# Optimization experiments

Hardware: AMD Instinct MI355X
Metric: run time of the kernel (lower is better)

Reference implementation:

```python
import jax, jax.numpy as jnp
import numpy as np

B, N, P = 8, 64, 128
DNODE, DEDGE, DEMB = 2048, 1024, 512
E = B * N * N


def setup_inputs() -> dict:
    key = jax.random.key(0)
    ks = jax.random.split(key, 12)
    x = jax.random.normal(ks[0], (B, N, DNODE), dtype=jnp.float32)
    interaction_feature = jax.random.normal(ks[1], (B, N, N, DEDGE), dtype=jnp.float32)
    s = 0.02
    W_phi = jax.random.normal(ks[2], (DNODE, DEMB), dtype=jnp.float32) * s
    b_phi = jax.random.normal(ks[3], (DEMB,), dtype=jnp.float32) * s
    W_psi = jax.random.normal(ks[4], (DNODE, DEMB), dtype=jnp.float32) * s
    b_psi = jax.random.normal(ks[5], (DEMB,), dtype=jnp.float32) * s
    W_node = jax.random.normal(ks[6], (DNODE, DEMB), dtype=jnp.float32) * s
    b_node = jax.random.normal(ks[7], (DEMB,), dtype=jnp.float32) * s
    W_rel = jax.random.normal(ks[8], (DEDGE, DEMB), dtype=jnp.float32) * s
    b_rel = jax.random.normal(ks[9], (DEMB,), dtype=jnp.float32) * s
    pairs = jax.random.randint(ks[10], (B, P, 2), 0, N, dtype=jnp.int32)
    # edge_locating_tensor: rows (batch, src, dst) covering the proposed edge set
    bb, ii, jj = jnp.meshgrid(jnp.arange(B), jnp.arange(N), jnp.arange(N), indexing='ij')
    edge_locating_tensor = jnp.stack([bb.ravel(), ii.ravel(), jj.ravel()], axis=1).astype(jnp.int32)  # [E,3]
    return {"x": x, "interaction_feature": interaction_feature, "W_phi": W_phi, "b_phi": b_phi,
            "W_psi": W_psi, "b_psi": b_psi, "W_node": W_node, "b_node": b_node,
            "W_rel": W_rel, "b_rel": b_rel, "pairs": pairs, "edge_locating_tensor": edge_locating_tensor}


def _lookup_edge(elt, b_idx, i0, i1):
    # boolean-mask argmax lookup, faithful to torch argmax(loc0*loc1*loc2)
    # elt: [E,3]; b_idx,i0,i1: [B,P] -> loc: [B,P] indices into edge list
    m = (elt[None, None, :, 0] == b_idx[:, :, None]) \
        & (elt[None, None, :, 1] == i0[:, :, None]) \
        & (elt[None, None, :, 2] == i1[:, :, None])  # [B,P,E]
    return jnp.argmax(m, axis=-1)


def reference(x, interaction_feature, W_phi, b_phi, W_psi, b_psi,
              W_node, b_node, W_rel, b_rel, pairs, edge_locating_tensor):
    # relationship proposal scoring: all-pairs einsum + sigmoid
    phi = x @ W_phi + b_phi                                    # [B,N,512]
    psi = x @ W_psi + b_psi                                    # [B,N,512]
    relatedness_score = jax.nn.sigmoid(jnp.einsum('bik,bjk->bij', phi, psi))  # [B,N,N]

    # node / relationship-node embedders
    node_emb = x @ W_node + b_node                             # [B,N,512]
    elt = edge_locating_tensor
    rel_feats = interaction_feature[elt[:, 0], elt[:, 1], elt[:, 2]]  # [E,1024] gather
    edge_emb = rel_feats @ W_rel + b_rel                       # [E,512]

    # classifier input construction (gather/argmax/scatter hot path, vectorized)
    ind0, ind1 = pairs[..., 0], pairs[..., 1]                  # [B,P]
    b_idx = jnp.broadcast_to(jnp.arange(B, dtype=jnp.int32)[:, None], ind0.shape)
    emb0 = node_emb[b_idx, ind0]                               # [B,P,512]
    emb1 = node_emb[b_idx, ind1]
    first_half = (emb0 + emb1) * 0.5                           # aggregate 'mean'

    loc_fwd = _lookup_edge(elt, b_idx, ind0, ind1)             # [B,P]
    loc_rev = _lookup_edge(elt, b_idx, ind1, ind0)
    e1 = edge_emb[loc_fwd]                                     # [B,P,512]
    e2 = edge_emb[loc_rev]
    second_half = (e1 + e2) * 0.5

    classifier_input = jnp.concatenate([first_half, second_half], axis=-1)  # [B,P,1024]
    return relatedness_score, classifier_input
```

## Files before the change

### kernel.cpp

```cpp
#include <hip/hip_runtime.h>
#include <hip/hip_bf16.h>


typedef _Float16 h16;
typedef h16 h16x4 __attribute__((ext_vector_type(4)));
typedef h16 h16x8 __attribute__((ext_vector_type(8)));
typedef float f32x4 __attribute__((ext_vector_type(4)));

static const long O_W3T  = 0;
static const long O_WREL = 6291456;
static const long O_XH   = 7340032;
static const long O_G    = 9437184;
static const long O_B3   = 11534336;
static const long O_YH   = 11540480;

__global__ __launch_bounds__(256) void k_prep(
    const float* __restrict__ Wphi, const float* __restrict__ Wpsi,
    const float* __restrict__ Wnode, const float* __restrict__ Wrel,
    const float* __restrict__ x, const float* __restrict__ bphi,
    const float* __restrict__ bpsi, const float* __restrict__ bnode,
    const float* __restrict__ feat, const int* __restrict__ pairs,
    h16* __restrict__ W3t, h16* __restrict__ Wrelt, h16* __restrict__ xh,
    float* __restrict__ b3, h16* __restrict__ G) {
  __shared__ float t[32][33];
  int bid = blockIdx.x, tid = threadIdx.x;
  if (bid < 3584) {
    const float* src; h16* dst; int K, tk, tn;
    if (bid < 3072) {
      int mat = bid >> 10, rem = bid & 1023;
      tk = rem >> 4; tn = rem & 15;
      src = mat == 0 ? Wphi : (mat == 1 ? Wpsi : Wnode);
      K = 2048; dst = W3t + (long)mat * 512 * 2048;
    } else {
      int rem = bid - 3072;
      tk = rem >> 4; tn = rem & 15;
      src = Wrel; K = 1024; dst = Wrelt;
    }
    {
      int row = tid >> 3, c4 = (tid & 7) * 4;
      float4 v = *(const float4*)(src + (long)(tk*32 + row)*512 + tn*32 + c4);
      t[row][c4+0] = v.x; t[row][c4+1] = v.y; t[row][c4+2] = v.z; t[row][c4+3] = v.w;
    }
    __syncthreads();
    {
      int n = tid >> 3, k4 = (tid & 7) * 4;
      h16x4 o = { (h16)t[k4+0][n], (h16)t[k4+1][n], (h16)t[k4+2][n], (h16)t[k4+3][n] };
      *(h16x4*)(dst + (long)(tn*32 + n)*K + tk*32 + k4) = o;
    }
  } else if (bid < 4102) {
    int b2 = bid - 3584;
    if (b2 < 512) {
      int idx = (b2*256 + tid) * 8;
      const float4* xv = (const float4*)(x + idx);
      float4 v0 = xv[0], v1 = xv[1];
      h16x8 o;
      o[0]=(h16)v0.x; o[1]=(h16)v0.y; o[2]=(h16)v0.z; o[3]=(h16)v0.w;
      o[4]=(h16)v1.x; o[5]=(h16)v1.y; o[6]=(h16)v1.z; o[7]=(h16)v1.w;
      *(h16x8*)(xh + idx) = o;
    } else {
      int i = (b2 - 512)*256 + tid;
      if (i < 1536) b3[i] = i < 512 ? bphi[i] : (i < 1024 ? bpsi[i-512] : bnode[i-1024]);
    }
  } else {
    int r = bid - 4102;
    int b = r >> 7;
    int i0 = pairs[r*2], i1 = pairs[r*2+1];
    const float4* f0 = (const float4*)(feat + (long)((b*64 + i0)*64 + i1) * 1024);
    const float4* f1 = (const float4*)(feat + (long)((b*64 + i1)*64 + i0) * 1024);
    float4 a = f0[tid], c = f1[tid];
    h16x4 o;
    o[0]=(h16)(0.5f*(a.x+c.x)); o[1]=(h16)(0.5f*(a.y+c.y));
    o[2]=(h16)(0.5f*(a.z+c.z)); o[3]=(h16)(0.5f*(a.w+c.w));
    *(h16x4*)(G + (long)r*1024 + tid*4) = o;
  }
}

__device__ __forceinline__ void mfma_compute(
    const h16 (*__restrict__ As)[72], const h16 (*__restrict__ Bs)[72],
    int wm, int wn, int fr, int kg, f32x4 acc[2][2]) {
#pragma unroll
  for (int kc = 0; kc < 2; ++kc) {
    int kb = kc*32 + kg;
    h16x8 fa0 = *(const h16x8*)&As[wm*32 + fr][kb];
    h16x8 fa1 = *(const h16x8*)&As[wm*32 + 16 + fr][kb];
    h16x8 fb0 = *(const h16x8*)&Bs[wn*32 + fr][kb];
    h16x8 fb1 = *(const h16x8*)&Bs[wn*32 + 16 + fr][kb];
    acc[0][0] = __builtin_amdgcn_mfma_f32_16x16x32_f16(fa0, fb0, acc[0][0], 0,0,0);
    acc[0][1] = __builtin_amdgcn_mfma_f32_16x16x32_f16(fa0, fb1, acc[0][1], 0,0,0);
    acc[1][0] = __builtin_amdgcn_mfma_f32_16x16x32_f16(fa1, fb0, acc[1][0], 0,0,0);
    acc[1][1] = __builtin_amdgcn_mfma_f32_16x16x32_f16(fa1, fb1, acc[1][1], 0,0,0);
  }
}

__device__ __forceinline__ void mfma_compute8(
    const h16 (*__restrict__ As)[72], const h16 (*__restrict__ Bs)[72],
    int wm, int wn, int fr, int kg, f32x4 acc[2]) {
#pragma unroll
  for (int kc = 0; kc < 2; ++kc) {
    int kb = kc*32 + kg;
    h16x8 fa0 = *(const h16x8*)&As[wm*32 + fr][kb];
    h16x8 fa1 = *(const h16x8*)&As[wm*32 + 16 + fr][kb];
    h16x8 fb  = *(const h16x8*)&Bs[wn*16 + fr][kb];
    acc[0] = __builtin_amdgcn_mfma_f32_16x16x32_f16(fa0, fb, acc[0], 0,0,0);
    acc[1] = __builtin_amdgcn_mfma_f32_16x16x32_f16(fa1, fb, acc[1], 0,0,0);
  }
}

#define BAR_LDS() { asm volatile("s_waitcnt lgkmcnt(0)" ::: "memory"); \
                    __builtin_amdgcn_s_barrier(); }

__global__ __launch_bounds__(512) void k_gemm(
    const h16* __restrict__ xh, const h16* __restrict__ W3t,
    const float* __restrict__ b3, h16* __restrict__ Yh,
    const h16* __restrict__ G, const h16* __restrict__ Wrelt,
    const float* __restrict__ brel, float* __restrict__ out) {
  __shared__ __align__(16) h16 As[2][64][72];
  __shared__ __align__(16) h16 Bs[2][64][72];
  int bid = blockIdx.x, tid = threadIdx.x;
  int lane = tid & 63, wave = tid >> 6;
  int wm = wave >> 2, wn = wave & 3;
  int srow = tid >> 3, skp = (tid & 7) * 8;
  int fr = lane & 15, kg = (lane >> 4) * 8;

  int isEdge = bid >= 192;
  int ntile = isEdge ? 2 : 1;
#pragma unroll 1
  for (int ti = 0; ti < ntile; ++ti) {
    if (ti) __syncthreads();
    const h16 *A, *Bt; int K, tileM, tileN;
    if (!isEdge) {
      A = xh; Bt = W3t; K = 2048;
      tileM = (bid / 24) * 64; tileN = (bid % 24) * 64;
    } else {
      int e = (bid - 192) * 2 + ti;
      A = G; Bt = Wrelt; K = 1024;
      tileM = (e >> 3) * 64; tileN = (e & 7) * 64;
    }
    const h16* Agp = A + (long)(tileM + srow) * K + skp;
    const h16* Bgp = Bt + (long)(tileN + srow) * K + skp;
    f32x4 acc[2] = {};

    h16x8 r0a = *(const h16x8*)(Agp);
    h16x8 r0b = *(const h16x8*)(Bgp);
    *(h16x8*)&As[0][srow][skp] = r0a;
    *(h16x8*)&Bs[0][srow][skp] = r0b;
    h16x8 ra1 = *(const h16x8*)(Agp + 64),  rb1 = *(const h16x8*)(Bgp + 64);
    h16x8 ra2 = *(const h16x8*)(Agp + 128), rb2 = *(const h16x8*)(Bgp + 128);
    BAR_LDS();
    int cur = 0;
#pragma unroll 1
    for (int k0 = 192; k0 < K; k0 += 64) {
      h16x8 raF = *(const h16x8*)(Agp + k0);
      h16x8 rbF = *(const h16x8*)(Bgp + k0);
      mfma_compute8(As[cur], Bs[cur], wm, wn, fr, kg, acc);
      *(h16x8*)&As[cur ^ 1][srow][skp] = ra1;
      *(h16x8*)&Bs[cur ^ 1][srow][skp] = rb1;
      BAR_LDS();
      ra1 = ra2; rb1 = rb2; ra2 = raF; rb2 = rbF;
      cur ^= 1;
    }
    mfma_compute8(As[cur], Bs[cur], wm, wn, fr, kg, acc);
    *(h16x8*)&As[cur ^ 1][srow][skp] = ra1;
    *(h16x8*)&Bs[cur ^ 1][srow][skp] = rb1;
    BAR_LDS();
    cur ^= 1;
    mfma_compute8(As[cur], Bs[cur], wm, wn, fr, kg, acc);
    *(h16x8*)&As[cur ^ 1][srow][skp] = ra2;
    *(h16x8*)&Bs[cur ^ 1][srow][skp] = rb2;
    BAR_LDS();
    cur ^= 1;
    mfma_compute8(As[cur], Bs[cur], wm, wn, fr, kg, acc);

    int r0 = 4 * (lane >> 4);
#pragma unroll
    for (int m = 0; m < 2; ++m) {
      int row = tileM + wm*32 + m*16 + r0;
      int col = tileN + wn*16 + fr;
      if (!isEdge) {
        float bb = b3[col];
#pragma unroll
        for (int r = 0; r < 4; ++r)
          Yh[(long)(row + r) * 1536 + col] = (h16)(acc[m][r] + bb);
      } else {
        float bb = brel[col];
#pragma unroll
        for (int r = 0; r < 4; ++r)
          out[32768 + 512 + (long)(row + r) * 1024 + col] = acc[m][r] + bb;
      }
    }
  }
}

#define GEMM_PIPELINE(Agp, Bgp, K)                                        \
  {                                                                       \
    h16x8 ra0 = *(const h16x8*)(Agp);                                     \
    h16x8 ra1 = *(const h16x8*)(Agp + 8);                                 \
    h16x8 rb0 = *(const h16x8*)(Bgp);                                     \
    h16x8 rb1 = *(const h16x8*)(Bgp + 8);                                 \
    *(h16x8*)&As[0][srow][skp]   = ra0;                                   \
    *(h16x8*)&As[0][srow][skp+8] = ra1;                                   \
    *(h16x8*)&Bs[0][srow][skp]   = rb0;                                   \
    *(h16x8*)&Bs[0][srow][skp+8] = rb1;                                   \
    __syncthreads();                                                      \
    int cur = 0;                                                          \
    for (int k0 = 64; k0 < (K); k0 += 64) {                               \
      ra0 = *(const h16x8*)(Agp + k0);                                    \
      ra1 = *(const h16x8*)(Agp + k0 + 8);                                \
      rb0 = *(const h16x8*)(Bgp + k0);                                    \
      rb1 = *(const h16x8*)(Bgp + k0 + 8);                                \
      mfma_compute(As[cur], Bs[cur], wm, wn, fr, kg, acc);                \
      int nxt = cur ^ 1;                                                  \
      *(h16x8*)&As[nxt][srow][skp]   = ra0;                               \
      *(h16x8*)&As[nxt][srow][skp+8] = ra1;                               \
      *(h16x8*)&Bs[nxt][srow][skp]   = rb0;                               \
      *(h16x8*)&Bs[nxt][srow][skp+8] = rb1;                               \
      __syncthreads();                                                    \
      cur = nxt;                                                          \
    }                                                                     \
    mfma_compute(As[cur], Bs[cur], wm, wn, fr, kg, acc);                  \
  }

__global__ __launch_bounds__(256) void k_epilogue(
    const h16* __restrict__ Yh, const int* __restrict__ pairs,
    float* __restrict__ out) {
  __shared__ __align__(16) h16 As[2][64][72];
  __shared__ __align__(16) h16 Bs[2][64][72];
  int bid = blockIdx.x, tid = threadIdx.x;
  if (bid < 8) {
    int lane = tid & 63, wave = tid >> 6;
    int wm = wave >> 1, wn = wave & 1;
    int srow = tid >> 2, skp = (tid & 3) * 16;
    int fr = lane & 15, kg = (lane >> 4) * 8;
    const h16* Ab = Yh + (long)bid * 64 * 1536;
    const h16* Agp = Ab + (long)srow * 1536 + skp;
    const h16* Bgp = Ab + (long)srow * 1536 + 512 + skp;
    f32x4 acc[2][2] = {};
    GEMM_PIPELINE(Agp, Bgp, 512);
    int r0 = 4 * (lane >> 4), c0 = lane & 15;
    float* ob = out + (long)bid * 4096;
#pragma unroll
    for (int m = 0; m < 2; ++m)
#pragma unroll
      for (int n = 0; n < 2; ++n) {
        int row = wm*32 + m*16 + r0;
        int col = wn*32 + n*16 + c0;
#pragma unroll
        for (int r = 0; r < 4; ++r) {
          float s = acc[m][n][r];
          ob[(long)(row + r) * 64 + col] = 1.f / (1.f + expf(-s));
        }
      }
  } else {
    int r = bid - 8;
    int b = r >> 7;
    int i0 = pairs[r*2], i1 = pairs[r*2+1];
    const h16* n0 = Yh + (long)(b*64 + i0)*1536 + 1024;
    const h16* n1 = Yh + (long)(b*64 + i1)*1536 + 1024;
    float* o = out + 32768 + (long)r*1024;
    for (int c = tid; c < 512; c += 256)
      o[c] = 0.5f*((float)n0[c] + (float)n1[c]);
  }
}

extern "C" void kernel_launch(void* const* d_in, const int* in_sizes, int n_in,
                              void* d_out, int out_size, void* d_ws, size_t ws_size,
                              hipStream_t stream) {
  const float* x     = (const float*)d_in[0];
  const float* feat  = (const float*)d_in[1];
  const float* Wphi  = (const float*)d_in[2];
  const float* bphi  = (const float*)d_in[3];
  const float* Wpsi  = (const float*)d_in[4];
  const float* bpsi  = (const float*)d_in[5];
  const float* Wnode = (const float*)d_in[6];
  const float* bnode = (const float*)d_in[7];
  const float* Wrel  = (const float*)d_in[8];
  const float* brel  = (const float*)d_in[9];
  const int*   pairs = (const int*)d_in[10];
  float* out = (float*)d_out;
  char* ws = (char*)d_ws;

  h16*   W3t   = (h16*)(ws + O_W3T);
  h16*   Wrelt = (h16*)(ws + O_WREL);
  h16*   xh    = (h16*)(ws + O_XH);
  h16*   G     = (h16*)(ws + O_G);
  float* b3    = (float*)(ws + O_B3);
  h16*   Yh    = (h16*)(ws + O_YH);

  k_prep<<<dim3(5126), dim3(256), 0, stream>>>(
      Wphi, Wpsi, Wnode, Wrel, x, bphi, bpsi, bnode, feat, pairs,
      W3t, Wrelt, xh, b3, G);
  k_gemm<<<dim3(256), dim3(512), 0, stream>>>(
      xh, W3t, b3, Yh, G, Wrelt, brel, out);
  k_epilogue<<<dim3(1032), dim3(256), 0, stream>>>(Yh, pairs, out);
}
```

Before: 34.80 us.

## Switch GEMM waves to intra-block split-K with LDS merge of partial accumulators

In the main GEMM and the relatedness einsum, the eight waves now form two K-slices of four waves each. Each wave computes a 32x32 sub-tile over half of every 64-wide K chunk instead of a 32x16 tile over the full chunk, which halves B-fragment reloads per MFMA. The two slices' partial sums are reduced through LDS before the epilogue. The einsum and gather epilogue kernel moves to 512 threads with the same split-K scheme. This adds two barriers and an LDS round trip per tile, and half the waves sit idle during the epilogue.

```diff
diff --git a/kernel.cpp b/kernel.cpp
--- a/kernel.cpp
+++ b/kernel.cpp
@@ -75,39 +75,80 @@
   }
 }
 
-__device__ __forceinline__ void mfma_compute(
+__device__ __forceinline__ void mfma4(
     const h16 (*__restrict__ As)[72], const h16 (*__restrict__ Bs)[72],
-    int wm, int wn, int fr, int kg, f32x4 acc[2][2]) {
-#pragma unroll
-  for (int kc = 0; kc < 2; ++kc) {
-    int kb = kc*32 + kg;
-    h16x8 fa0 = *(const h16x8*)&As[wm*32 + fr][kb];
-    h16x8 fa1 = *(const h16x8*)&As[wm*32 + 16 + fr][kb];
-    h16x8 fb0 = *(const h16x8*)&Bs[wn*32 + fr][kb];
-    h16x8 fb1 = *(const h16x8*)&Bs[wn*32 + 16 + fr][kb];
-    acc[0][0] = __builtin_amdgcn_mfma_f32_16x16x32_f16(fa0, fb0, acc[0][0], 0,0,0);
-    acc[0][1] = __builtin_amdgcn_mfma_f32_16x16x32_f16(fa0, fb1, acc[0][1], 0,0,0);
-    acc[1][0] = __builtin_amdgcn_mfma_f32_16x16x32_f16(fa1, fb0, acc[1][0], 0,0,0);
-    acc[1][1] = __builtin_amdgcn_mfma_f32_16x16x32_f16(fa1, fb1, acc[1][1], 0,0,0);
-  }
-}
-
-__device__ __forceinline__ void mfma_compute8(
-    const h16 (*__restrict__ As)[72], const h16 (*__restrict__ Bs)[72],
-    int wm, int wn, int fr, int kg, f32x4 acc[2]) {
-#pragma unroll
-  for (int kc = 0; kc < 2; ++kc) {
-    int kb = kc*32 + kg;
-    h16x8 fa0 = *(const h16x8*)&As[wm*32 + fr][kb];
-    h16x8 fa1 = *(const h16x8*)&As[wm*32 + 16 + fr][kb];
-    h16x8 fb  = *(const h16x8*)&Bs[wn*16 + fr][kb];
-    acc[0] = __builtin_amdgcn_mfma_f32_16x16x32_f16(fa0, fb, acc[0], 0,0,0);
-    acc[1] = __builtin_amdgcn_mfma_f32_16x16x32_f16(fa1, fb, acc[1], 0,0,0);
-  }
+    int wm, int wn, int kb, int fr, f32x4 acc[2][2]) {
+  h16x8 fa0 = *(const h16x8*)&As[wm*32 + fr][kb];
+  h16x8 fa1 = *(const h16x8*)&As[wm*32 + 16 + fr][kb];
+  h16x8 fb0 = *(const h16x8*)&Bs[wn*32 + fr][kb];
+  h16x8 fb1 = *(const h16x8*)&Bs[wn*32 + 16 + fr][kb];
+  acc[0][0] = __builtin_amdgcn_mfma_f32_16x16x32_f16(fa0, fb0, acc[0][0], 0,0,0);
+  acc[0][1] = __builtin_amdgcn_mfma_f32_16x16x32_f16(fa0, fb1, acc[0][1], 0,0,0);
+  acc[1][0] = __builtin_amdgcn_mfma_f32_16x16x32_f16(fa1, fb0, acc[1][0], 0,0,0);
+  acc[1][1] = __builtin_amdgcn_mfma_f32_16x16x32_f16(fa1, fb1, acc[1][1], 0,0,0);
 }
 
 #define BAR_LDS() { asm volatile("s_waitcnt lgkmcnt(0)" ::: "memory"); \
                     __builtin_amdgcn_s_barrier(); }
+
+template<int S>
+__device__ __forceinline__ void tile_splitk(
+    const h16* Agp, const h16* Bgp,
+    h16 (*As)[64][72], h16 (*Bs)[64][72],
+    int srow, int skp, int wm, int wn, int kb, int fr,
+    f32x4 acc[2][2]) {
+  h16x8 r0a = *(const h16x8*)(Agp);
+  h16x8 r0b = *(const h16x8*)(Bgp);
+  *(h16x8*)&As[0][srow][skp] = r0a;
+  *(h16x8*)&Bs[0][srow][skp] = r0b;
+  h16x8 ra1 = *(const h16x8*)(Agp + 64),  rb1 = *(const h16x8*)(Bgp + 64);
+  h16x8 ra2 = *(const h16x8*)(Agp + 128), rb2 = *(const h16x8*)(Bgp + 128);
+  BAR_LDS();
+  int cur = 0;
+#pragma unroll 1
+  for (int k0 = 192; k0 < S * 64; k0 += 64) {
+    h16x8 raF = *(const h16x8*)(Agp + k0);
+    h16x8 rbF = *(const h16x8*)(Bgp + k0);
+    mfma4(As[cur], Bs[cur], wm, wn, kb, fr, acc);
+    *(h16x8*)&As[cur ^ 1][srow][skp] = ra1;
+    *(h16x8*)&Bs[cur ^ 1][srow][skp] = rb1;
+    BAR_LDS();
+    ra1 = ra2; rb1 = rb2; ra2 = raF; rb2 = rbF;
+    cur ^= 1;
+  }
+  mfma4(As[cur], Bs[cur], wm, wn, kb, fr, acc);
+  *(h16x8*)&As[cur ^ 1][srow][skp] = ra1;
+  *(h16x8*)&Bs[cur ^ 1][srow][skp] = rb1;
+  BAR_LDS();
+  cur ^= 1;
+  mfma4(As[cur], Bs[cur], wm, wn, kb, fr, acc);
+  *(h16x8*)&As[cur ^ 1][srow][skp] = ra2;
+  *(h16x8*)&Bs[cur ^ 1][srow][skp] = rb2;
+  BAR_LDS();
+  cur ^= 1;
+  mfma4(As[cur], Bs[cur], wm, wn, kb, fr, acc);
+}
+
+__device__ __forceinline__ void splitk_merge(
+    h16 (*As)[64][72], int wave, int lane, f32x4 acc[2][2]) {
+  float* mb = (float*)As;
+  __syncthreads();
+  if (wave >= 4) {
+    int mi = ((wave - 4) * 64 + lane) * 16;
+    *(f32x4*)&mb[mi +  0] = acc[0][0];
+    *(f32x4*)&mb[mi +  4] = acc[0][1];
+    *(f32x4*)&mb[mi +  8] = acc[1][0];
+    *(f32x4*)&mb[mi + 12] = acc[1][1];
+  }
+  __syncthreads();
+  if (wave < 4) {
+    int mi = (wave * 64 + lane) * 16;
+    acc[0][0] += *(const f32x4*)&mb[mi +  0];
+    acc[0][1] += *(const f32x4*)&mb[mi +  4];
+    acc[1][0] += *(const f32x4*)&mb[mi +  8];
+    acc[1][1] += *(const f32x4*)&mb[mi + 12];
+  }
+}
 
 __global__ __launch_bounds__(512) void k_gemm(
     const h16* __restrict__ xh, const h16* __restrict__ W3t,
@@ -118,9 +159,11 @@
   __shared__ __align__(16) h16 Bs[2][64][72];
   int bid = blockIdx.x, tid = threadIdx.x;
   int lane = tid & 63, wave = tid >> 6;
-  int wm = wave >> 2, wn = wave & 3;
+  int kslice = wave >> 2, wsub = wave & 3;
+  int wm = wsub >> 1, wn = wsub & 1;
   int srow = tid >> 3, skp = (tid & 7) * 8;
-  int fr = lane & 15, kg = (lane >> 4) * 8;
+  int fr = lane & 15, kb = kslice * 32 + (lane >> 4) * 8;
+  int r0 = 4 * (lane >> 4), c0 = lane & 15;
 
   int isEdge = bid >= 192;
   int ntile = isEdge ? 2 : 1;
@@ -138,89 +181,35 @@
     }
     const h16* Agp = A + (long)(tileM + srow) * K + skp;
     const h16* Bgp = Bt + (long)(tileN + srow) * K + skp;
-    f32x4 acc[2] = {};
-
-    h16x8 r0a = *(const h16x8*)(Agp);
-    h16x8 r0b = *(const h16x8*)(Bgp);
-    *(h16x8*)&As[0][srow][skp] = r0a;
-    *(h16x8*)&Bs[0][srow][skp] = r0b;
-    h16x8 ra1 = *(const h16x8*)(Agp + 64),  rb1 = *(const h16x8*)(Bgp + 64);
-    h16x8 ra2 = *(const h16x8*)(Agp + 128), rb2 = *(const h16x8*)(Bgp + 128);
-    BAR_LDS();
-    int cur = 0;
-#pragma unroll 1
-    for (int k0 = 192; k0 < K; k0 += 64) {
-      h16x8 raF = *(const h16x8*)(Agp + k0);
-      h16x8 rbF = *(const h16x8*)(Bgp + k0);
-      mfma_compute8(As[cur], Bs[cur], wm, wn, fr, kg, acc);
-      *(h16x8*)&As[cur ^ 1][srow][skp] = ra1;
-      *(h16x8*)&Bs[cur ^ 1][srow][skp] = rb1;
-      BAR_LDS();
-      ra1 = ra2; rb1 = rb2; ra2 = raF; rb2 = rbF;
-      cur ^= 1;
-    }
-    mfma_compute8(As[cur], Bs[cur], wm, wn, fr, kg, acc);
-    *(h16x8*)&As[cur ^ 1][srow][skp] = ra1;
-    *(h16x8*)&Bs[cur ^ 1][srow][skp] = rb1;
-    BAR_LDS();
-    cur ^= 1;
-    mfma_compute8(As[cur], Bs[cur], wm, wn, fr, kg, acc);
-    *(h16x8*)&As[cur ^ 1][srow][skp] = ra2;
-    *(h16x8*)&Bs[cur ^ 1][srow][skp] = rb2;
-    BAR_LDS();
-    cur ^= 1;
-    mfma_compute8(As[cur], Bs[cur], wm, wn, fr, kg, acc);
-
-    int r0 = 4 * (lane >> 4);
-#pragma unroll
-    for (int m = 0; m < 2; ++m) {
-      int row = tileM + wm*32 + m*16 + r0;
-      int col = tileN + wn*16 + fr;
-      if (!isEdge) {
-        float bb = b3[col];
-#pragma unroll
-        for (int r = 0; r < 4; ++r)
-          Yh[(long)(row + r) * 1536 + col] = (h16)(acc[m][r] + bb);
-      } else {
-        float bb = brel[col];
-#pragma unroll
-        for (int r = 0; r < 4; ++r)
-          out[32768 + 512 + (long)(row + r) * 1024 + col] = acc[m][r] + bb;
-      }
-    }
-  }
-}
-
-#define GEMM_PIPELINE(Agp, Bgp, K)                                        \
-  {                                                                       \
-    h16x8 ra0 = *(const h16x8*)(Agp);                                     \
-    h16x8 ra1 = *(const h16x8*)(Agp + 8);                                 \
-    h16x8 rb0 = *(const h16x8*)(Bgp);                                     \
-    h16x8 rb1 = *(const h16x8*)(Bgp + 8);                                 \
-    *(h16x8*)&As[0][srow][skp]   = ra0;                                   \
-    *(h16x8*)&As[0][srow][skp+8] = ra1;                                   \
-    *(h16x8*)&Bs[0][srow][skp]   = rb0;                                   \
-    *(h16x8*)&Bs[0][srow][skp+8] = rb1;                                   \
-    __syncthreads();                                                      \
-    int cur = 0;                                                          \
-    for (int k0 = 64; k0 < (K); k0 += 64) {                               \
-      ra0 = *(const h16x8*)(Agp + k0);                                    \
-      ra1 = *(const h16x8*)(Agp + k0 + 8);                                \
-      rb0 = *(const h16x8*)(Bgp + k0);                                    \
-      rb1 = *(const h16x8*)(Bgp + k0 + 8);                                \
-      mfma_compute(As[cur], Bs[cur], wm, wn, fr, kg, acc);                \
-      int nxt = cur ^ 1;                                                  \
-      *(h16x8*)&As[nxt][srow][skp]   = ra0;                               \
-      *(h16x8*)&As[nxt][srow][skp+8] = ra1;                               \
-      *(h16x8*)&Bs[nxt][srow][skp]   = rb0;                               \
-      *(h16x8*)&Bs[nxt][srow][skp+8] = rb1;                               \
-      __syncthreads();                                                    \
-      cur = nxt;                                                          \
-    }                                                                     \
-    mfma_compute(As[cur], Bs[cur], wm, wn, fr, kg, acc);                  \
-  }
-
-__global__ __launch_bounds__(256) void k_epilogue(
+    f32x4 acc[2][2] = {};
+    if (!isEdge) tile_splitk<32>(Agp, Bgp, As, Bs, srow, skp, wm, wn, kb, fr, acc);
+    else         tile_splitk<16>(Agp, Bgp, As, Bs, srow, skp, wm, wn, kb, fr, acc);
+    splitk_merge(As, wave, lane, acc);
+
+    if (wave < 4) {
+#pragma unroll
+      for (int m = 0; m < 2; ++m)
+#pragma unroll
+        for (int n = 0; n < 2; ++n) {
+          int row = tileM + wm*32 + m*16 + r0;
+          int col = tileN + wn*32 + n*16 + c0;
+          if (!isEdge) {
+            float bb = b3[col];
+#pragma unroll
+            for (int r = 0; r < 4; ++r)
+              Yh[(long)(row + r) * 1536 + col] = (h16)(acc[m][n][r] + bb);
+          } else {
+            float bb = brel[col];
+#pragma unroll
+            for (int r = 0; r < 4; ++r)
+              out[32768 + 512 + (long)(row + r) * 1024 + col] = acc[m][n][r] + bb;
+          }
+        }
+    }
+  }
+}
+
+__global__ __launch_bounds__(512) void k_epilogue(
     const h16* __restrict__ Yh, const int* __restrict__ pairs,
     float* __restrict__ out) {
   __shared__ __align__(16) h16 As[2][64][72];
@@ -228,28 +217,32 @@
   int bid = blockIdx.x, tid = threadIdx.x;
   if (bid < 8) {
     int lane = tid & 63, wave = tid >> 6;
-    int wm = wave >> 1, wn = wave & 1;
-    int srow = tid >> 2, skp = (tid & 3) * 16;
-    int fr = lane & 15, kg = (lane >> 4) * 8;
+    int kslice = wave >> 2, wsub = wave & 3;
+    int wm = wsub >> 1, wn = wsub & 1;
+    int srow = tid >> 3, skp = (tid & 7) * 8;
+    int fr = lane & 15, kb = kslice * 32 + (lane >> 4) * 8;
     const h16* Ab = Yh + (long)bid * 64 * 1536;
     const h16* Agp = Ab + (long)srow * 1536 + skp;
     const h16* Bgp = Ab + (long)srow * 1536 + 512 + skp;
     f32x4 acc[2][2] = {};
-    GEMM_PIPELINE(Agp, Bgp, 512);
-    int r0 = 4 * (lane >> 4), c0 = lane & 15;
-    float* ob = out + (long)bid * 4096;
-#pragma unroll
-    for (int m = 0; m < 2; ++m)
-#pragma unroll
-      for (int n = 0; n < 2; ++n) {
-        int row = wm*32 + m*16 + r0;
-        int col = wn*32 + n*16 + c0;
-#pragma unroll
-        for (int r = 0; r < 4; ++r) {
-          float s = acc[m][n][r];
-          ob[(long)(row + r) * 64 + col] = 1.f / (1.f + expf(-s));
+    tile_splitk<8>(Agp, Bgp, As, Bs, srow, skp, wm, wn, kb, fr, acc);
+    splitk_merge(As, wave, lane, acc);
+    if (wave < 4) {
+      int r0 = 4 * (lane >> 4), c0 = lane & 15;
+      float* ob = out + (long)bid * 4096;
+#pragma unroll
+      for (int m = 0; m < 2; ++m)
+#pragma unroll
+        for (int n = 0; n < 2; ++n) {
+          int row = wm*32 + m*16 + r0;
+          int col = wn*32 + n*16 + c0;
+#pragma unroll
+          for (int r = 0; r < 4; ++r) {
+            float s = acc[m][n][r];
+            ob[(long)(row + r) * 64 + col] = 1.f / (1.f + expf(-s));
+          }
         }
-      }
+    }
   } else {
     int r = bid - 8;
     int b = r >> 7;
@@ -257,8 +250,8 @@
     const h16* n0 = Yh + (long)(b*64 + i0)*1536 + 1024;
     const h16* n1 = Yh + (long)(b*64 + i1)*1536 + 1024;
     float* o = out + 32768 + (long)r*1024;
-    for (int c = tid; c < 512; c += 256)
-      o[c] = 0.5f*((float)n0[c] + (float)n1[c]);
+    if (tid < 512)
+      o[tid] = 0.5f*((float)n0[tid] + (float)n1[tid]);
   }
 }
 
@@ -291,5 +284,5 @@
       W3t, Wrelt, xh, b3, G);
   k_gemm<<<dim3(256), dim3(512), 0, stream>>>(
       xh, W3t, b3, Yh, G, Wrelt, brel, out);
-  k_epilogue<<<dim3(1032), dim3(256), 0, stream>>>(Yh, pairs, out);
-}
+  k_epilogue<<<dim3(1032), dim3(512), 0, stream>>>(Yh, pairs, out);
+}
```

New measurement: 33.79 us. 1.03x faster.
